# Kernel optimization log

Hardware: AMD Instinct MI355X
Metric: run time of the kernel (lower is better)

Reference implementation:

```python
import jax, jax.numpy as jnp
import numpy as np

PAD_IND = 3
SOS_IND = 0
NSTEPS = 25
H = 256   # hidden_size
D = 256   # input_size (embedding dim)
L = 3     # lstm_layers


def _lstm_cell(x, h, c, Wih, Whh, bih, bhh):
    # torch LSTM gate order: i, f, g, o
    g = x @ Wih.T + bih + h @ Whh.T + bhh
    i, f, gg, o = jnp.split(g, 4, axis=-1)
    c2 = jax.nn.sigmoid(f) * c + jax.nn.sigmoid(i) * jnp.tanh(gg)
    h2 = jax.nn.sigmoid(o) * jnp.tanh(c2)
    return h2, c2


def setup_inputs() -> dict:
    key = jax.random.key(0)
    ks = jax.random.split(key, 24)
    B, T = 64, 256
    Vin, C = 32000, 32000
    s = 1.0 / np.sqrt(H)

    def u(k, shape):
        return jax.random.uniform(k, shape, jnp.float32, -s, s)

    return dict(
        x=jax.random.randint(ks[0], (B, T), 0, Vin),
        target_val=jax.random.randint(ks[1], (B, NSTEPS), 0, C),
        enc_embed=jax.random.normal(ks[2], (Vin, D), jnp.float32),
        enc_Wih=u(ks[3], (L, 4 * H, D)),
        enc_Whh=u(ks[4], (L, 4 * H, H)),
        enc_bih=u(ks[5], (L, 4 * H)),
        enc_bhh=u(ks[6], (L, 4 * H)),
        Wq=u(ks[7], (H, H)), bq=u(ks[8], (H,)),
        Wk=u(ks[9], (H, H)), bk=u(ks[10], (H,)),
        Wv=u(ks[11], (H, H)), bv=u(ks[12], (H,)),
        Wo=u(ks[13], (H, H)), bo=u(ks[14], (H,)),
        dec_embed=jax.random.normal(ks[15], (C, D), jnp.float32),
        dec_Wih0=u(ks[16], (4 * H, 2 * H)),            # decoder layer 0 input is [emb; ctx] = 2H
        dec_Wih_rest=u(ks[17], (L - 1, 4 * H, H)),
        dec_Whh=u(ks[18], (L, 4 * H, H)),
        dec_bih=u(ks[19], (L, 4 * H)),
        dec_bhh=u(ks[20], (L, 4 * H)),
        dec_W=u(ks[21], (C, H)),
        dec_b=u(ks[22], (C,)),
    )


def reference(x, target_val, enc_embed, enc_Wih, enc_Whh, enc_bih, enc_bhh,
              Wq, bq, Wk, bk, Wv, bv, Wo, bo,
              dec_embed, dec_Wih0, dec_Wih_rest, dec_Whh, dec_bih, dec_bhh,
              dec_W, dec_b):
    B, T = x.shape
    lengths = (x != PAD_IND).sum(axis=1)            # [B], emulates pack_padded_sequence
    emb = enc_embed[x]                              # [B,T,D]
    valid = (jnp.arange(T)[:, None] < lengths[None, :])[..., None]  # [T,B,1]
    h0 = jnp.zeros((L, B, H), emb.dtype)
    c0 = jnp.zeros((L, B, H), emb.dtype)

    def enc_step(carry, inp):
        h, c = carry
        xt, v = inp
        hs, cs = [], []
        z = xt
        for l in range(L):
            hl, cl = _lstm_cell(z, h[l], c[l], enc_Wih[l], enc_Whh[l], enc_bih[l], enc_bhh[l])
            hl = jnp.where(v, hl, h[l])             # freeze state past sequence length
            cl = jnp.where(v, cl, c[l])
            hs.append(hl); cs.append(cl)
            z = hl
        h = jnp.stack(hs); c = jnp.stack(cs)
        return (h, c), jnp.where(v, h[-1], 0.0)     # pad_packed pads with zeros

    (enc_h, enc_c), outs = jax.lax.scan(enc_step, (h0, c0), (jnp.swapaxes(emb, 0, 1), valid))
    enc_hiddens = jnp.swapaxes(outs, 0, 1)          # [B,T,H]

    # attention key/value projections are loop-invariant -> hoist out of decode loop
    kp = enc_hiddens @ Wk.T + bk                    # [B,T,H]
    vp = enc_hiddens @ Wv.T + bv                    # [B,T,H]
    scale = 1.0 / jnp.sqrt(jnp.asarray(H, emb.dtype))
    dec_Wih = [dec_Wih0, dec_Wih_rest[0], dec_Wih_rest[1]]
    tok0 = jnp.full((B,), SOS_IND, jnp.int32)

    def dec_step(carry, _):
        h, c, tok = carry
        e = dec_embed[tok]                          # [B,D]
        q = h.sum(axis=0) @ Wq.T + bq               # prev_state[0].sum(axis=0) -> [B,H]
        scores = jnp.einsum('bh,bth->bt', q, kp) * scale
        attn = jax.nn.softmax(scores, axis=-1)
        ctx = jnp.einsum('bt,bth->bh', attn, vp) @ Wo.T + bo
        z = jnp.concatenate([e, ctx], axis=-1)      # [B,2H]
        hs, cs = [], []
        for l in range(L):
            hl, cl = _lstm_cell(z, h[l], c[l], dec_Wih[l], dec_Whh[l], dec_bih[l], dec_bhh[l])
            hs.append(hl); cs.append(cl)
            z = hl
        h = jnp.stack(hs); c = jnp.stack(cs)
        logits = z @ dec_W.T + dec_b                # [B,C]
        tok = jnp.argmax(logits, axis=-1).astype(jnp.int32)  # greedy feedback (TF ratio = 0)
        return (h, c, tok), logits

    _, logits = jax.lax.scan(dec_step, (enc_h, enc_c, tok0), None, length=NSTEPS)  # [25,B,C]
    return jnp.swapaxes(logits, 0, 1)[:, :, None, :]  # [B,25,1,C] like the torch module
```

## Files before the change

kernel.cpp:

```cpp
#include <hip/hip_runtime.h>
#include <math.h>

#define TT    256
#define NB    64
#define HH    256
#define NSTEP 25
#define NCLS  32000
#define PADI  3

__device__ __align__(16) float g_hring[3][2][NB][HH];
__device__ __align__(16) float g_enchid[TT][NB][HH];
__device__ __align__(16) float g_kp[NB][TT][HH];
__device__ __align__(16) float g_vp[NB][TT][HH];
__device__ __align__(16) float g_cfin[3][NB][HH];
__device__ __align__(16) float g_hdec[2][3][NB][HH];
__device__ __align__(16) float g_z0[NB][512];
__device__ float    g_wmax[256][NB];
__device__ int      g_wmaxi[256][NB];
__device__ int      g_len[NB];
__device__ unsigned g_arrive[256];
__device__ unsigned g_release;

__global__ void k_zero_flags(){
  g_arrive[threadIdx.x] = 0u;
  if (threadIdx.x == 0) g_release = 0u;
}

__device__ __forceinline__ float sigf(float v){ return 1.0f / (1.0f + expf(-v)); }

#define SCOPE_AG __HIP_MEMORY_SCOPE_AGENT
typedef unsigned long long u64;
__device__ __forceinline__ float2 ld2(const float* p){
  u64 v = __hip_atomic_load((const u64*)p, __ATOMIC_RELAXED, SCOPE_AG);
  float2 r; __builtin_memcpy(&r, &v, 8); return r;
}
__device__ __forceinline__ void st2(float* p, float2 f){
  u64 v; __builtin_memcpy(&v, &f, 8);
  __hip_atomic_store((u64*)p, v, __ATOMIC_RELAXED, SCOPE_AG);
}
__device__ __forceinline__ float ldc(const float* p){ return __hip_atomic_load(p, __ATOMIC_RELAXED, SCOPE_AG); }
__device__ __forceinline__ void  stc(float* p, float v){ __hip_atomic_store(p, v, __ATOMIC_RELAXED, SCOPE_AG); }
__device__ __forceinline__ int   ldi(const int* p){ return __hip_atomic_load(p, __ATOMIC_RELAXED, SCOPE_AG); }
__device__ __forceinline__ void  sti(int* p, int v){ __hip_atomic_store(p, v, __ATOMIC_RELAXED, SCOPE_AG); }
__device__ __forceinline__ unsigned ldu(const unsigned* p){ return __hip_atomic_load(p, __ATOMIC_RELAXED, SCOPE_AG); }
__device__ __forceinline__ void  stu(unsigned* p, unsigned v){ __hip_atomic_store(p, v, __ATOMIC_RELAXED, SCOPE_AG); }

#define DOT4(a_, x_, w_) (a_) += (x_).x*(w_).x + (x_).y*(w_).y + (x_).z*(w_).z + (x_).w*(w_).w

#define WENC(cb,g,jj,u) (((((cb)*12+(g))*8+(jj))*36)+(u))

__device__ __forceinline__ void gbar(int w, unsigned target){
  asm volatile("s_waitcnt vmcnt(0)" ::: "memory");
  __syncthreads();
  if (threadIdx.x == 0) stu(&g_arrive[w], target);
  if (w == 0){
    if (threadIdx.x < 64){
      const int i4 = threadIdx.x * 4;
      for (;;){
        unsigned a0 = ldu(&g_arrive[i4+0]);
        unsigned a1 = ldu(&g_arrive[i4+1]);
        unsigned a2 = ldu(&g_arrive[i4+2]);
        unsigned a3 = ldu(&g_arrive[i4+3]);
        if (__all((a0>=target) && (a1>=target) && (a2>=target) && (a3>=target))) break;
        __builtin_amdgcn_s_sleep(1);
      }
      if (threadIdx.x == 0) stu(&g_release, target);
    }
  } else {
    if (threadIdx.x == 0){
      while (ldu(&g_release) < target) __builtin_amdgcn_s_sleep(2);
    }
  }
  __syncthreads();
}

template<int NCB, int BASE>
__device__ __forceinline__ void dec_gates(const float* sw, const float* i0, const float* i1,
                                          const float* i2, int j, float out4[4]){
  float a0=0.f, a1=0.f, a2=0.f, a3=0.f;
  const float* ips[3] = { i0, i1, i2 };
  #pragma unroll
  for (int cb = 0; cb < NCB; ++cb){
    float2 xin[16];
    #pragma unroll
    for (int u = 0; u < 16; ++u) xin[u] = ld2(ips[cb] + u*16 + 2*j);
    #pragma unroll
    for (int u2 = 0; u2 < 8; ++u2){
      float2 pa = xin[2*u2], pb = xin[2*u2+1];
      const float* wb = &sw[BASE + (((cb*4+0)*8+j)*36) + u2*4];
      float4 w0 = *(const float4*)(wb);
      float4 w1 = *(const float4*)(wb + 288);
      float4 w2 = *(const float4*)(wb + 576);
      float4 w3 = *(const float4*)(wb + 864);
      a0 += pa.x*w0.x + pa.y*w0.y + pb.x*w0.z + pb.y*w0.w;
      a1 += pa.x*w1.x + pa.y*w1.y + pb.x*w1.z + pb.y*w1.w;
      a2 += pa.x*w2.x + pa.y*w2.y + pb.x*w2.z + pb.y*w2.w;
      a3 += pa.x*w3.x + pa.y*w3.y + pb.x*w3.z + pb.y*w3.w;
    }
  }
  #pragma unroll
  for (int m = 1; m < 8; m <<= 1){
    a0 += __shfl_xor(a0, m); a1 += __shfl_xor(a1, m);
    a2 += __shfl_xor(a2, m); a3 += __shfl_xor(a3, m);
  }
  out4[0]=a0; out4[1]=a1; out4[2]=a2; out4[3]=a3;
}

__global__ void __launch_bounds__(512, 1)
k_main(const int*   __restrict__ p_x,
       const float* __restrict__ p_eemb,
       const float* __restrict__ p_eWih,  const float* __restrict__ p_eWhh,
       const float* __restrict__ p_ebih,  const float* __restrict__ p_ebhh,
       const float* __restrict__ p_Wq, const float* __restrict__ p_bq,
       const float* __restrict__ p_Wk, const float* __restrict__ p_bk,
       const float* __restrict__ p_Wv, const float* __restrict__ p_bv,
       const float* __restrict__ p_Wo, const float* __restrict__ p_bo,
       const float* __restrict__ p_demb,
       const float* __restrict__ p_dWih0, const float* __restrict__ p_dWihR,
       const float* __restrict__ p_dWhh,
       const float* __restrict__ p_dbih,  const float* __restrict__ p_dbhh,
       const float* __restrict__ p_dW,    const float* __restrict__ p_db,
       float* __restrict__ p_out)
{
  __shared__ __align__(16) float s_w[8064];
  __shared__ __align__(16) float s_h2[NB*HH];
  __shared__ float s_benc[12];
  __shared__ float s_bdec[12];
  __shared__ __align__(16) float s_hs[256];
  __shared__ __align__(16) float s_q[256];
  __shared__ __align__(16) float s_sc[256];
  __shared__ __align__(16) float s_at[256];
  __shared__ __align__(16) float s_ctx[256];
  __shared__ float s_rv[8];  __shared__ int s_ri[8];
  __shared__ float s_rv2[8][16]; __shared__ int s_ri2[8][16];

  const int w   = blockIdx.x;
  const int tid = threadIdx.x;
  const int b   = tid >> 3;
  const int j   = tid & 7;
  unsigned bar  = 0;

  const int lay0 = (w < 255) ? (w / 85) : 0;
  const int h0   = (w < 255) ? ((w - lay0*85) * 3) : 0;

  for (int fi = tid; fi < 6144; fi += 512){
    int g = fi >> 9, k = fi & 511;
    int e = g >> 2, gt = g & 3;
    int l   = (w < 255) ? lay0 : e;
    int hh2 = (w < 255) ? (h0 + e) : 255;
    int row = gt*256 + hh2;
    float v = (k < 256) ? p_eWih[((size_t)l*1024 + row)*256 + k]
                        : p_eWhh[((size_t)l*1024 + row)*256 + (k - 256)];
    int cb = k >> 8, kk = k & 255;
    s_w[WENC(cb, g, (kk & 15) >> 1, ((kk >> 4) << 1) | (kk & 1))] = v;
  }
  if (tid < 12){
    int e = tid >> 2, gt = tid & 3;
    int l   = (w < 255) ? lay0 : e;
    int hh2 = (w < 255) ? (h0 + e) : 255;
    int row = gt*256 + hh2;
    s_benc[tid] = p_ebih[l*1024 + row] + p_ebhh[l*1024 + row];
  }
  if (w < 64){
    int cnt = 0;
    if (tid < 256) cnt = (p_x[w*TT + tid] != PADI) ? 1 : 0;
    #pragma unroll
    for (int m = 1; m < 64; m <<= 1) cnt += __shfl_xor(cnt, m);
    if ((tid & 63) == 0) s_ri[tid >> 6] = cnt;
    __syncthreads();
    if (tid == 0){ int t2 = 0; for (int q2 = 0; q2 < 8; ++q2) t2 += s_ri[q2]; sti(&g_len[w], t2); }
  }
  if (tid < 192){
    int fi = w*192 + tid;
    int l = fi >> 14, rem = fi & 16383;
    stc(&g_hring[l][1][rem >> 8][rem & 255], 0.f);
  }
  gbar(w, ++bar);

  const int len_b = ldi(&g_len[b]);

  float c_reg[3] = {0.f,0.f,0.f};
  float h_reg[3] = {0.f,0.f,0.f};

  for (int sdiag = 0; sdiag < TT + 2; ++sdiag){
    float acc[12];
    #pragma unroll
    for (int g = 0; g < 12; ++g) acc[g] = 0.f;

    if (w < 255){
      const int t = sdiag - lay0;
      if (t >= 0 && t < TT){
        float2 x2[16], h2[16];
        if (lay0 == 0){
          const float* xs = p_eemb + (size_t)p_x[b*TT + t]*HH;
          #pragma unroll
          for (int u = 0; u < 16; ++u) x2[u] = *(const float2*)(xs + u*16 + 2*j);
        } else {
          const float* xs = &g_hring[lay0-1][t & 1][b][0];
          #pragma unroll
          for (int u = 0; u < 16; ++u) x2[u] = ld2(xs + u*16 + 2*j);
        }
        {
          const float* hsv = &g_hring[lay0][(t & 1) ^ 1][b][0];
          #pragma unroll
          for (int u = 0; u < 16; ++u) h2[u] = ld2(hsv + u*16 + 2*j);
        }
        #pragma unroll
        for (int u2 = 0; u2 < 8; ++u2){
          float2 xa = x2[2*u2], xb = x2[2*u2+1];
          float2 ha = h2[2*u2], hb = h2[2*u2+1];
          #pragma unroll
          for (int g = 0; g < 12; ++g){
            float4 wx = *(const float4*)&s_w[WENC(0, g, j, u2*4)];
            float4 wh = *(const float4*)&s_w[WENC(1, g, j, u2*4)];
            acc[g] += xa.x*wx.x + xa.y*wx.y + xb.x*wx.z + xb.y*wx.w
                    + ha.x*wh.x + ha.y*wh.y + hb.x*wh.z + hb.y*wh.w;
          }
        }
      }
    } else {
      #pragma unroll
      for (int e = 0; e < 3; ++e){
        const int t = sdiag - e;
        if (t >= 0 && t < TT){
          float2 x2[16], h2[16];
          if (e == 0){
            const float* xs = p_eemb + (size_t)p_x[b*TT + t]*HH;
            #pragma unroll
            for (int u = 0; u < 16; ++u) x2[u] = *(const float2*)(xs + u*16 + 2*j);
          } else {
            const float* xs = &g_hring[e-1][t & 1][b][0];
            #pragma unroll
            for (int u = 0; u < 16; ++u) x2[u] = ld2(xs + u*16 + 2*j);
          }
          {
            const float* hsv = &g_hring[e][(t & 1) ^ 1][b][0];
            #pragma unroll
            for (int u = 0; u < 16; ++u) h2[u] = ld2(hsv + u*16 + 2*j);
          }
          #pragma unroll
          for (int u2 = 0; u2 < 8; ++u2){
            float2 xa = x2[2*u2], xb = x2[2*u2+1];
            float2 ha = h2[2*u2], hb = h2[2*u2+1];
            #pragma unroll
            for (int g2 = 0; g2 < 4; ++g2){
              float4 wx = *(const float4*)&s_w[WENC(0, e*4+g2, j, u2*4)];
              float4 wh = *(const float4*)&s_w[WENC(1, e*4+g2, j, u2*4)];
              acc[e*4+g2] += xa.x*wx.x + xa.y*wx.y + xb.x*wx.z + xb.y*wx.w
                           + ha.x*wh.x + ha.y*wh.y + hb.x*wh.z + hb.y*wh.w;
            }
          }
        }
      }
    }

    #pragma unroll
    for (int g = 0; g < 12; ++g){
      float v = acc[g];
      v += __shfl_xor(v, 1); v += __shfl_xor(v, 2); v += __shfl_xor(v, 4);
      acc[g] = v;
    }

    if (j == 0){
      #pragma unroll
      for (int e = 0; e < 3; ++e){
        const int lay = (w < 255) ? lay0 : e;
        const int hh2 = (w < 255) ? (h0 + e) : 255;
        const int t = sdiag - lay;
        if (t >= 0 && t < TT){
          float iv = acc[e*4+0] + s_benc[e*4+0];
          float fv = acc[e*4+1] + s_benc[e*4+1];
          float gv = acc[e*4+2] + s_benc[e*4+2];
          float ov = acc[e*4+3] + s_benc[e*4+3];
          float c2 = sigf(fv)*c_reg[e] + sigf(iv)*tanhf(gv);
          float h2v = sigf(ov)*tanhf(c2);
          bool valid = (t < len_b);
          if (valid){ c_reg[e] = c2; h_reg[e] = h2v; }
          stc(&g_hring[lay][t & 1][b][hh2], h_reg[e]);
          if (lay == 2) stc(&g_enchid[t][b][hh2], valid ? h_reg[e] : 0.f);
        }
      }
    }
    gbar(w, ++bar);
  }

  if (j == 0){
    #pragma unroll
    for (int e = 0; e < 3; ++e){
      const int lay = (w < 255) ? lay0 : e;
      const int hh2 = (w < 255) ? (h0 + e) : 255;
      stc(&g_cfin[lay][b][hh2], c_reg[e]);
    }
  }
  gbar(w, ++bar);

  {
    const int b2 = w >> 2, t0 = (w & 3) * 64;
    const int n1 = tid & 127, rq = tid >> 7;
    for (int p = 0; p < 4; ++p){
      const int n = p*128 + n1;
      const float* wrow = (n < 256) ? (p_Wk + (size_t)n*HH) : (p_Wv + (size_t)(n-256)*HH);
      const float bias  = (n < 256) ? p_bk[n] : p_bv[n-256];
      const float4* wr4 = (const float4*)wrow;
      const float* hb = &g_enchid[t0 + rq*16][b2][0];
      const float4* hr[16];
      #pragma unroll
      for (int r = 0; r < 16; ++r) hr[r] = (const float4*)(hb + (size_t)r*NB*HH);
      float a16[16];
      #pragma unroll
      for (int r = 0; r < 16; ++r) a16[r] = 0.f;
      for (int k4 = 0; k4 < 64; ++k4){
        float4 wv = wr4[k4];
        #pragma unroll
        for (int r = 0; r < 16; ++r){ float4 h4 = hr[r][k4]; DOT4(a16[r], h4, wv); }
      }
      float* orow = (n < 256) ? &g_kp[b2][t0 + rq*16][n] : &g_vp[b2][t0 + rq*16][n-256];
      #pragma unroll
      for (int r = 0; r < 16; ++r) stc(orow + (size_t)r*HH, a16[r] + bias);
    }
  }

  for (int fi = tid; fi < 3072; fi += 512){
    int g = fi / 768, k = fi % 768; int row = g*256 + w;
    float v = (k < 512) ? p_dWih0[(size_t)row*512 + k]
                        : p_dWhh[(size_t)row*HH + (k - 512)];
    int cb = k >> 8, kk = k & 255;
    s_w[(((cb*4 + g)*8 + ((kk & 15) >> 1))*36) + (((kk >> 4) << 1) | (kk & 1))] = v;
  }
  for (int fi = tid; fi < 2048; fi += 512){
    int g = fi / 512, k = fi % 512; int row = g*256 + w;
    float v = (k < 256) ? p_dWihR[(size_t)row*HH + k]
                        : p_dWhh[(size_t)(1024 + row)*HH + (k - 256)];
    int cb = k >> 8, kk = k & 255;
    s_w[3456 + (((cb*4 + g)*8 + ((kk & 15) >> 1))*36) + (((kk >> 4) << 1) | (kk & 1))] = v;
  }
  for (int fi = tid; fi < 2048; fi += 512){
    int g = fi / 512, k = fi % 512; int row = g*256 + w;
    float v = (k < 256) ? p_dWihR[(size_t)(1024 + row)*HH + k]
                        : p_dWhh[(size_t)(2048 + row)*HH + (k - 256)];
    int cb = k >> 8, kk = k & 255;
    s_w[5760 + (((cb*4 + g)*8 + ((kk & 15) >> 1))*36) + (((kk >> 4) << 1) | (kk & 1))] = v;
  }
  if (tid < 12){
    int l = tid >> 2, g = tid & 3; int row = g*256 + w;
    s_bdec[tid] = p_dbih[l*1024 + row] + p_dbhh[l*1024 + row];
  }
  gbar(w, ++bar);

  if (tid < 192){
    int fi = w*192 + tid;
    int l = fi >> 14, rem = fi & 16383;
    stc(&g_hdec[0][l][rem >> 8][rem & 255], ldc(&g_hring[l][1][rem >> 8][rem & 255]));
  }
  float c_d0 = 0.f, c_d1 = 0.f, c_d2 = 0.f;
  if (j == 0){
    c_d0 = ldc(&g_cfin[0][b][w]); c_d1 = ldc(&g_cfin[1][b][w]); c_d2 = ldc(&g_cfin[2][b][w]);
  }
  gbar(w, ++bar);

  for (int st = 0; st < NSTEP; ++st){
    const int slot = st & 1, nxt = slot ^ 1;

    if (w < 64){
      const int bA = w;
      int tok = 0;
      if (st > 0){
        float v = -1e38f; int idx = 0;
        if (tid < 256){ v = ldc(&g_wmax[tid][bA]); idx = ldi(&g_wmaxi[tid][bA]); }
        #pragma unroll
        for (int m = 1; m < 64; m <<= 1){
          float ov = __shfl_xor(v, m); int oi = __shfl_xor(idx, m);
          if (ov > v || (ov == v && oi < idx)){ v = ov; idx = oi; }
        }
        if ((tid & 63) == 0){ s_rv[tid >> 6] = v; s_ri[tid >> 6] = idx; }
        __syncthreads();
        if (tid == 0){
          float bv2 = s_rv[0]; int bi2 = s_ri[0];
          for (int q2 = 1; q2 < 8; ++q2){
            float ov = s_rv[q2]; int oi = s_ri[q2];
            if (ov > bv2 || (ov == bv2 && oi < bi2)){ bv2 = ov; bi2 = oi; }
          }
          s_ri[0] = bi2;
        }
        __syncthreads();
        tok = s_ri[0];
      }
      if (tid < 256)
        s_hs[tid] = ldc(&g_hdec[slot][0][bA][tid]) + ldc(&g_hdec[slot][1][bA][tid])
                  + ldc(&g_hdec[slot][2][bA][tid]);
      __syncthreads();
      if (tid < 256){
        float a = p_bq[tid];
        const float4* wr = (const float4*)(p_Wq + (size_t)tid*HH);
        #pragma unroll 8
        for (int k4 = 0; k4 < 64; ++k4){
          float4 wv = wr[k4]; float4 h4 = *(const float4*)&s_hs[k4*4]; DOT4(a, h4, wv);
        }
        s_q[tid] = a;
      }
      __syncthreads();
      if (tid < 256){
        float a = 0.f;
        const float4* kr = (const float4*)&g_kp[bA][tid][0];
        #pragma unroll 8
        for (int k4 = 0; k4 < 64; ++k4){
          float4 kv = kr[k4]; float4 q4 = *(const float4*)&s_q[k4*4]; DOT4(a, q4, kv);
        }
        s_sc[tid] = a * 0.0625f;
      }
      __syncthreads();
      {
        float sv = (tid < 256) ? s_sc[tid] : -1e38f;
        float m2 = sv;
        #pragma unroll
        for (int m = 1; m < 64; m <<= 1) m2 = fmaxf(m2, __shfl_xor(m2, m));
        if ((tid & 63) == 0) s_rv[tid >> 6] = m2;
        __syncthreads();
        if (tid == 0){ float mm = s_rv[0]; for (int q2 = 1; q2 < 8; ++q2) mm = fmaxf(mm, s_rv[q2]); s_rv[0] = mm; }
        __syncthreads();
        const float mx = s_rv[0];
        float ev = (tid < 256) ? expf(sv - mx) : 0.f;
        float ss = ev;
        #pragma unroll
        for (int m = 1; m < 64; m <<= 1) ss += __shfl_xor(ss, m);
        __syncthreads();
        if ((tid & 63) == 0) s_rv[tid >> 6] = ss;
        __syncthreads();
        if (tid == 0){ float t2 = 0.f; for (int q2 = 0; q2 < 8; ++q2) t2 += s_rv[q2]; s_rv[0] = t2; }
        __syncthreads();
        if (tid < 256) s_at[tid] = ev / s_rv[0];
      }
      __syncthreads();
      if (tid < 256){
        float a = 0.f;
        const float* vb = &g_vp[bA][0][tid];
        #pragma unroll 4
        for (int t4 = 0; t4 < 64; ++t4){
          float4 a4 = *(const float4*)&s_at[t4*4];
          a += a4.x*vb[(size_t)(t4*4+0)*HH] + a4.y*vb[(size_t)(t4*4+1)*HH]
             + a4.z*vb[(size_t)(t4*4+2)*HH] + a4.w*vb[(size_t)(t4*4+3)*HH];
        }
        s_ctx[tid] = a;
      }
      __syncthreads();
      if (tid < 256){
        float a = p_bo[tid];
        const float4* wr = (const float4*)(p_Wo + (size_t)tid*HH);
        #pragma unroll 8
        for (int k4 = 0; k4 < 64; ++k4){
          float4 wv = wr[k4]; float4 c4 = *(const float4*)&s_ctx[k4*4]; DOT4(a, c4, wv);
        }
        stc(&g_z0[bA][256 + tid], a);
        stc(&g_z0[bA][tid], p_demb[(size_t)tok*HH + tid]);
      }
    }
    gbar(w, ++bar);

    {
      float g4[4];
      dec_gates<3, 0>(s_w, &g_z0[b][0], &g_z0[b][256], &g_hdec[slot][0][b][0], j, g4);
      if (j == 0){
        float iv = g4[0]+s_bdec[0], fv = g4[1]+s_bdec[1], gv = g4[2]+s_bdec[2], ov = g4[3]+s_bdec[3];
        float c2 = sigf(fv)*c_d0 + sigf(iv)*tanhf(gv); c_d0 = c2;
        stc(&g_hdec[nxt][0][b][w], sigf(ov)*tanhf(c2));
      }
    }
    gbar(w, ++bar);
    {
      float g4[4];
      dec_gates<2, 3456>(s_w, &g_hdec[nxt][0][b][0], &g_hdec[slot][1][b][0], nullptr, j, g4);
      if (j == 0){
        float iv = g4[0]+s_bdec[4], fv = g4[1]+s_bdec[5], gv = g4[2]+s_bdec[6], ov = g4[3]+s_bdec[7];
        float c2 = sigf(fv)*c_d1 + sigf(iv)*tanhf(gv); c_d1 = c2;
        stc(&g_hdec[nxt][1][b][w], sigf(ov)*tanhf(c2));
      }
    }
    gbar(w, ++bar);
    {
      float g4[4];
      dec_gates<2, 5760>(s_w, &g_hdec[nxt][1][b][0], &g_hdec[slot][2][b][0], nullptr, j, g4);
      if (j == 0){
        float iv = g4[0]+s_bdec[8], fv = g4[1]+s_bdec[9], gv = g4[2]+s_bdec[10], ov = g4[3]+s_bdec[11];
        float c2 = sigf(fv)*c_d2 + sigf(iv)*tanhf(gv); c_d2 = c2;
        stc(&g_hdec[nxt][2][b][w], sigf(ov)*tanhf(c2));
      }
    }
    gbar(w, ++bar);

    {
      {
        const float* src = &g_hdec[nxt][2][0][0];
        #pragma unroll
        for (int u = 0; u < 16; ++u){
          int fo = 2*(tid + 512*u);
          float2 v = ld2(src + fo);
          *(float2*)(s_h2 + fo) = v;
        }
      }
      __syncthreads();

      const int cq = tid & 127, qb = tid >> 7;
      const bool cok = (cq < 125);
      const int c  = w*125 + cq;
      const int cc = cok ? c : (w*125);
      const float4* wr = (const float4*)(p_dW + (size_t)cc*HH);
      const float4* zr[16];
      #pragma unroll
      for (int r = 0; r < 16; ++r) zr[r] = (const float4*)&s_h2[(qb*16 + r)*HH];
      float a16[16];
      #pragma unroll
      for (int r = 0; r < 16; ++r) a16[r] = 0.f;
      for (int k4 = 0; k4 < 64; ++k4){
        float4 wv = wr[k4];
        #pragma unroll
        for (int r = 0; r < 16; ++r){ float4 z4 = zr[r][k4]; DOT4(a16[r], z4, wv); }
      }
      const float bias = cok ? p_db[cc] : 0.f;
      #pragma unroll
      for (int r = 0; r < 16; ++r){
        const int bb = qb*16 + r;
        float val = a16[r] + bias;
        if (cok) p_out[((size_t)bb*NSTEP + st)*NCLS + c] = val;
        float v = cok ? val : -1e38f;
        int idx = cok ? c : 0x7fffffff;
        #pragma unroll
        for (int m = 1; m < 64; m <<= 1){
          float ov = __shfl_xor(v, m); int oi = __shfl_xor(idx, m);
          if (ov > v || (ov == v && oi < idx)){ v = ov; idx = oi; }
        }
        if ((tid & 63) == 0){ s_rv2[tid >> 6][r] = v; s_ri2[tid >> 6][r] = idx; }
      }
      __syncthreads();
      if (tid < 64){
        const int qb2 = tid >> 4, r = tid & 15;
        float v1 = s_rv2[qb2*2][r];   int i1 = s_ri2[qb2*2][r];
        float v2 = s_rv2[qb2*2+1][r]; int i2 = s_ri2[qb2*2+1][r];
        bool take2 = (v2 > v1) || (v2 == v1 && i2 < i1);
        stc(&g_wmax[w][qb2*16 + r],  take2 ? v2 : v1);
        sti(&g_wmaxi[w][qb2*16 + r], take2 ? i2 : i1);
      }
      __syncthreads();
    }
    gbar(w, ++bar);
  }
}

extern "C" void kernel_launch(void* const* d_in, const int* in_sizes, int n_in,
                              void* d_out, int out_size, void* d_ws, size_t ws_size,
                              hipStream_t stream){
  (void)in_sizes; (void)n_in; (void)out_size; (void)d_ws; (void)ws_size;
  const int*   x     = (const int*)d_in[0];
  const float* eemb  = (const float*)d_in[2];
  const float* eWih  = (const float*)d_in[3];
  const float* eWhh  = (const float*)d_in[4];
  const float* ebih  = (const float*)d_in[5];
  const float* ebhh  = (const float*)d_in[6];
  const float* Wq    = (const float*)d_in[7];
  const float* bq    = (const float*)d_in[8];
  const float* Wk    = (const float*)d_in[9];
  const float* bk    = (const float*)d_in[10];
  const float* Wv    = (const float*)d_in[11];
  const float* bv    = (const float*)d_in[12];
  const float* Wo    = (const float*)d_in[13];
  const float* bo    = (const float*)d_in[14];
  const float* demb  = (const float*)d_in[15];
  const float* dWih0 = (const float*)d_in[16];
  const float* dWihR = (const float*)d_in[17];
  const float* dWhh  = (const float*)d_in[18];
  const float* dbih  = (const float*)d_in[19];
  const float* dbhh  = (const float*)d_in[20];
  const float* dW    = (const float*)d_in[21];
  const float* db    = (const float*)d_in[22];
  float* out = (float*)d_out;

  k_zero_flags<<<dim3(1), dim3(256), 0, stream>>>();
  k_main<<<dim3(256), dim3(512), 0, stream>>>(
      x, eemb, eWih, eWhh, ebih, ebhh,
      Wq, bq, Wk, bk, Wv, bv, Wo, bo,
      demb, dWih0, dWihR, dWhh, dbih, dbhh, dW, db, out);
}
```

Before: 5.994 ms.

## Register-block encoder cells over two batches and rebalance output projection tiling

The encoder recurrence now gives each thread two batch rows and 16 k-lanes, so every shared-memory weight float4 is reused across two batches. Weights are stored in a plain contiguous layout, and the 768 hidden-unit slots are split evenly across blocks, so blocks at a layer boundary can straddle two layers. The decoder output projection computes two classes by eight batch rows per thread and reduces the argmax within a wavefront, which removes the LDS reduction stage and two syncthreads. The barrier spin sleep is also shortened, and the change adds shuffle steps and register pressure in exchange.

```diff
diff --git a/kernel.cpp b/kernel.cpp
--- a/kernel.cpp
+++ b/kernel.cpp
@@ -34,10 +34,6 @@
   u64 v = __hip_atomic_load((const u64*)p, __ATOMIC_RELAXED, SCOPE_AG);
   float2 r; __builtin_memcpy(&r, &v, 8); return r;
 }
-__device__ __forceinline__ void st2(float* p, float2 f){
-  u64 v; __builtin_memcpy(&v, &f, 8);
-  __hip_atomic_store((u64*)p, v, __ATOMIC_RELAXED, SCOPE_AG);
-}
 __device__ __forceinline__ float ldc(const float* p){ return __hip_atomic_load(p, __ATOMIC_RELAXED, SCOPE_AG); }
 __device__ __forceinline__ void  stc(float* p, float v){ __hip_atomic_store(p, v, __ATOMIC_RELAXED, SCOPE_AG); }
 __device__ __forceinline__ int   ldi(const int* p){ return __hip_atomic_load(p, __ATOMIC_RELAXED, SCOPE_AG); }
@@ -46,8 +42,6 @@
 __device__ __forceinline__ void  stu(unsigned* p, unsigned v){ __hip_atomic_store(p, v, __ATOMIC_RELAXED, SCOPE_AG); }
 
 #define DOT4(a_, x_, w_) (a_) += (x_).x*(w_).x + (x_).y*(w_).y + (x_).z*(w_).z + (x_).w*(w_).w
-
-#define WENC(cb,g,jj,u) (((((cb)*12+(g))*8+(jj))*36)+(u))
 
 __device__ __forceinline__ void gbar(int w, unsigned target){
   asm volatile("s_waitcnt vmcnt(0)" ::: "memory");
@@ -68,7 +62,7 @@
     }
   } else {
     if (threadIdx.x == 0){
-      while (ldu(&g_release) < target) __builtin_amdgcn_s_sleep(2);
+      while (ldu(&g_release) < target) __builtin_amdgcn_s_sleep(1);
     }
   }
   __syncthreads();
@@ -132,7 +126,6 @@
   __shared__ __align__(16) float s_at[256];
   __shared__ __align__(16) float s_ctx[256];
   __shared__ float s_rv[8];  __shared__ int s_ri[8];
-  __shared__ float s_rv2[8][16]; __shared__ int s_ri2[8][16];
 
   const int w   = blockIdx.x;
   const int tid = threadIdx.x;
@@ -140,25 +133,26 @@
   const int j   = tid & 7;
   unsigned bar  = 0;
 
-  const int lay0 = (w < 255) ? (w / 85) : 0;
-  const int h0   = (w < 255) ? ((w - lay0*85) * 3) : 0;
+  const int b2  = tid >> 4;
+  const int je  = tid & 15;
+  const int slot3 = 3*w;
+  const int layU  = slot3 >> 8;
+  const bool uni  = ((slot3 + 2) >> 8) == layU;
 
   for (int fi = tid; fi < 6144; fi += 512){
-    int g = fi >> 9, k = fi & 511;
-    int e = g >> 2, gt = g & 3;
-    int l   = (w < 255) ? lay0 : e;
-    int hh2 = (w < 255) ? (h0 + e) : 255;
-    int row = gt*256 + hh2;
-    float v = (k < 256) ? p_eWih[((size_t)l*1024 + row)*256 + k]
-                        : p_eWhh[((size_t)l*1024 + row)*256 + (k - 256)];
-    int cb = k >> 8, kk = k & 255;
-    s_w[WENC(cb, g, (kk & 15) >> 1, ((kk >> 4) << 1) | (kk & 1))] = v;
+    int cb = fi / 3072, rem = fi - cb*3072;
+    int g = rem >> 8, k = rem & 255;
+    int s3 = slot3 + (g >> 2);
+    int l = s3 >> 8, hh = s3 & 255;
+    int row = (g & 3)*256 + hh;
+    float v = (cb == 0) ? p_eWih[((size_t)l*1024 + row)*256 + k]
+                        : p_eWhh[((size_t)l*1024 + row)*256 + k];
+    s_w[fi] = v;
   }
   if (tid < 12){
-    int e = tid >> 2, gt = tid & 3;
-    int l   = (w < 255) ? lay0 : e;
-    int hh2 = (w < 255) ? (h0 + e) : 255;
-    int row = gt*256 + hh2;
+    int s3 = slot3 + (tid >> 2);
+    int l = s3 >> 8, hh = s3 & 255;
+    int row = (tid & 3)*256 + hh;
     s_benc[tid] = p_ebih[l*1024 + row] + p_ebhh[l*1024 + row];
   }
   if (w < 64){
@@ -177,77 +171,113 @@
   }
   gbar(w, ++bar);
 
-  const int len_b = ldi(&g_len[b]);
-
-  float c_reg[3] = {0.f,0.f,0.f};
-  float h_reg[3] = {0.f,0.f,0.f};
+  const int len0 = ldi(&g_len[2*b2]);
+  const int len1 = ldi(&g_len[2*b2+1]);
+
+  float c_reg[3][2] = {{0.f,0.f},{0.f,0.f},{0.f,0.f}};
+  float h_reg[3][2] = {{0.f,0.f},{0.f,0.f},{0.f,0.f}};
 
   for (int sdiag = 0; sdiag < TT + 2; ++sdiag){
-    float acc[12];
+    float acc[12][2];
     #pragma unroll
-    for (int g = 0; g < 12; ++g) acc[g] = 0.f;
-
-    if (w < 255){
-      const int t = sdiag - lay0;
+    for (int g = 0; g < 12; ++g){ acc[g][0] = 0.f; acc[g][1] = 0.f; }
+
+    if (uni){
+      const int t = sdiag - layU;
       if (t >= 0 && t < TT){
-        float2 x2[16], h2[16];
-        if (lay0 == 0){
-          const float* xs = p_eemb + (size_t)p_x[b*TT + t]*HH;
+        float4 xv[2][4], hv[2][4];
+        #pragma unroll
+        for (int bb = 0; bb < 2; ++bb){
+          const int batch = 2*b2 + bb;
+          const float* hs = &g_hring[layU][(t & 1) ^ 1][batch][0];
+          if (layU == 0){
+            const float* xs = p_eemb + (size_t)p_x[batch*TT + t]*HH;
+            #pragma unroll
+            for (int u = 0; u < 4; ++u){
+              int off = 64*u + 4*je;
+              float2 a = *(const float2*)(xs + off);
+              float2 c = *(const float2*)(xs + off + 2);
+              xv[bb][u] = make_float4(a.x, a.y, c.x, c.y);
+            }
+          } else {
+            const float* xs = &g_hring[layU-1][t & 1][batch][0];
+            #pragma unroll
+            for (int u = 0; u < 4; ++u){
+              int off = 64*u + 4*je;
+              float2 a = ld2(xs + off), c = ld2(xs + off + 2);
+              xv[bb][u] = make_float4(a.x, a.y, c.x, c.y);
+            }
+          }
           #pragma unroll
-          for (int u = 0; u < 16; ++u) x2[u] = *(const float2*)(xs + u*16 + 2*j);
-        } else {
-          const float* xs = &g_hring[lay0-1][t & 1][b][0];
-          #pragma unroll
-          for (int u = 0; u < 16; ++u) x2[u] = ld2(xs + u*16 + 2*j);
-        }
-        {
-          const float* hsv = &g_hring[lay0][(t & 1) ^ 1][b][0];
-          #pragma unroll
-          for (int u = 0; u < 16; ++u) h2[u] = ld2(hsv + u*16 + 2*j);
-        }
-        #pragma unroll
-        for (int u2 = 0; u2 < 8; ++u2){
-          float2 xa = x2[2*u2], xb = x2[2*u2+1];
-          float2 ha = h2[2*u2], hb = h2[2*u2+1];
+          for (int u = 0; u < 4; ++u){
+            int off = 64*u + 4*je;
+            float2 a = ld2(hs + off), c = ld2(hs + off + 2);
+            hv[bb][u] = make_float4(a.x, a.y, c.x, c.y);
+          }
+        }
+        #pragma unroll
+        for (int u = 0; u < 4; ++u){
           #pragma unroll
           for (int g = 0; g < 12; ++g){
-            float4 wx = *(const float4*)&s_w[WENC(0, g, j, u2*4)];
-            float4 wh = *(const float4*)&s_w[WENC(1, g, j, u2*4)];
-            acc[g] += xa.x*wx.x + xa.y*wx.y + xb.x*wx.z + xb.y*wx.w
-                    + ha.x*wh.x + ha.y*wh.y + hb.x*wh.z + hb.y*wh.w;
+            float4 wx = *(const float4*)&s_w[g*256 + 64*u + 4*je];
+            float4 wh = *(const float4*)&s_w[3072 + g*256 + 64*u + 4*je];
+            #pragma unroll
+            for (int bb = 0; bb < 2; ++bb){
+              DOT4(acc[g][bb], xv[bb][u], wx);
+              DOT4(acc[g][bb], hv[bb][u], wh);
+            }
           }
         }
       }
     } else {
       #pragma unroll
       for (int e = 0; e < 3; ++e){
-        const int t = sdiag - e;
+        const int s3 = slot3 + e;
+        const int lay = s3 >> 8;
+        const int t = sdiag - lay;
         if (t >= 0 && t < TT){
-          float2 x2[16], h2[16];
-          if (e == 0){
-            const float* xs = p_eemb + (size_t)p_x[b*TT + t]*HH;
+          float4 xv[2][4], hv[2][4];
+          #pragma unroll
+          for (int bb = 0; bb < 2; ++bb){
+            const int batch = 2*b2 + bb;
+            const float* hs = &g_hring[lay][(t & 1) ^ 1][batch][0];
+            if (lay == 0){
+              const float* xs = p_eemb + (size_t)p_x[batch*TT + t]*HH;
+              #pragma unroll
+              for (int u = 0; u < 4; ++u){
+                int off = 64*u + 4*je;
+                float2 a = *(const float2*)(xs + off);
+                float2 c = *(const float2*)(xs + off + 2);
+                xv[bb][u] = make_float4(a.x, a.y, c.x, c.y);
+              }
+            } else {
+              const float* xs = &g_hring[lay-1][t & 1][batch][0];
+              #pragma unroll
+              for (int u = 0; u < 4; ++u){
+                int off = 64*u + 4*je;
+                float2 a = ld2(xs + off), c = ld2(xs + off + 2);
+                xv[bb][u] = make_float4(a.x, a.y, c.x, c.y);
+              }
+            }
             #pragma unroll
-            for (int u = 0; u < 16; ++u) x2[u] = *(const float2*)(xs + u*16 + 2*j);
-          } else {
-            const float* xs = &g_hring[e-1][t & 1][b][0];
-            #pragma unroll
-            for (int u = 0; u < 16; ++u) x2[u] = ld2(xs + u*16 + 2*j);
-          }
-          {
-            const float* hsv = &g_hring[e][(t & 1) ^ 1][b][0];
-            #pragma unroll
-            for (int u = 0; u < 16; ++u) h2[u] = ld2(hsv + u*16 + 2*j);
+            for (int u = 0; u < 4; ++u){
+              int off = 64*u + 4*je;
+              float2 a = ld2(hs + off), c = ld2(hs + off + 2);
+              hv[bb][u] = make_float4(a.x, a.y, c.x, c.y);
+            }
           }
           #pragma unroll
-          for (int u2 = 0; u2 < 8; ++u2){
-            float2 xa = x2[2*u2], xb = x2[2*u2+1];
-            float2 ha = h2[2*u2], hb = h2[2*u2+1];
+          for (int u = 0; u < 4; ++u){
             #pragma unroll
-            for (int g2 = 0; g2 < 4; ++g2){
-              float4 wx = *(const float4*)&s_w[WENC(0, e*4+g2, j, u2*4)];
-              float4 wh = *(const float4*)&s_w[WENC(1, e*4+g2, j, u2*4)];
-              acc[e*4+g2] += xa.x*wx.x + xa.y*wx.y + xb.x*wx.z + xb.y*wx.w
-                           + ha.x*wh.x + ha.y*wh.y + hb.x*wh.z + hb.y*wh.w;
+            for (int gt = 0; gt < 4; ++gt){
+              int g = e*4 + gt;
+              float4 wx = *(const float4*)&s_w[g*256 + 64*u + 4*je];
+              float4 wh = *(const float4*)&s_w[3072 + g*256 + 64*u + 4*je];
+              #pragma unroll
+              for (int bb = 0; bb < 2; ++bb){
+                DOT4(acc[g][bb], xv[bb][u], wx);
+                DOT4(acc[g][bb], hv[bb][u], wh);
+              }
             }
           }
         }
@@ -256,53 +286,62 @@
 
     #pragma unroll
     for (int g = 0; g < 12; ++g){
-      float v = acc[g];
-      v += __shfl_xor(v, 1); v += __shfl_xor(v, 2); v += __shfl_xor(v, 4);
-      acc[g] = v;
-    }
-
-    if (j == 0){
+      #pragma unroll
+      for (int bb = 0; bb < 2; ++bb){
+        float v = acc[g][bb];
+        v += __shfl_xor(v, 1); v += __shfl_xor(v, 2);
+        v += __shfl_xor(v, 4); v += __shfl_xor(v, 8);
+        acc[g][bb] = v;
+      }
+    }
+
+    if (je == 0){
       #pragma unroll
       for (int e = 0; e < 3; ++e){
-        const int lay = (w < 255) ? lay0 : e;
-        const int hh2 = (w < 255) ? (h0 + e) : 255;
+        const int s3 = slot3 + e;
+        const int lay = s3 >> 8, hh = s3 & 255;
         const int t = sdiag - lay;
         if (t >= 0 && t < TT){
-          float iv = acc[e*4+0] + s_benc[e*4+0];
-          float fv = acc[e*4+1] + s_benc[e*4+1];
-          float gv = acc[e*4+2] + s_benc[e*4+2];
-          float ov = acc[e*4+3] + s_benc[e*4+3];
-          float c2 = sigf(fv)*c_reg[e] + sigf(iv)*tanhf(gv);
-          float h2v = sigf(ov)*tanhf(c2);
-          bool valid = (t < len_b);
-          if (valid){ c_reg[e] = c2; h_reg[e] = h2v; }
-          stc(&g_hring[lay][t & 1][b][hh2], h_reg[e]);
-          if (lay == 2) stc(&g_enchid[t][b][hh2], valid ? h_reg[e] : 0.f);
+          #pragma unroll
+          for (int bb = 0; bb < 2; ++bb){
+            const int batch = 2*b2 + bb;
+            float iv = acc[e*4+0][bb] + s_benc[e*4+0];
+            float fv = acc[e*4+1][bb] + s_benc[e*4+1];
+            float gv = acc[e*4+2][bb] + s_benc[e*4+2];
+            float ov = acc[e*4+3][bb] + s_benc[e*4+3];
+            float c2 = sigf(fv)*c_reg[e][bb] + sigf(iv)*tanhf(gv);
+            float h2v = sigf(ov)*tanhf(c2);
+            bool valid = (t < ((bb == 0) ? len0 : len1));
+            if (valid){ c_reg[e][bb] = c2; h_reg[e][bb] = h2v; }
+            stc(&g_hring[lay][t & 1][batch][hh], h_reg[e][bb]);
+            if (lay == 2) stc(&g_enchid[t][batch][hh], valid ? h_reg[e][bb] : 0.f);
+          }
         }
       }
     }
     gbar(w, ++bar);
   }
 
-  if (j == 0){
+  if (je == 0){
     #pragma unroll
     for (int e = 0; e < 3; ++e){
-      const int lay = (w < 255) ? lay0 : e;
-      const int hh2 = (w < 255) ? (h0 + e) : 255;
-      stc(&g_cfin[lay][b][hh2], c_reg[e]);
+      const int s3 = slot3 + e;
+      const int lay = s3 >> 8, hh = s3 & 255;
+      stc(&g_cfin[lay][2*b2][hh],   c_reg[e][0]);
+      stc(&g_cfin[lay][2*b2+1][hh], c_reg[e][1]);
     }
   }
   gbar(w, ++bar);
 
   {
-    const int b2 = w >> 2, t0 = (w & 3) * 64;
+    const int b3 = w >> 2, t0 = (w & 3) * 64;
     const int n1 = tid & 127, rq = tid >> 7;
     for (int p = 0; p < 4; ++p){
       const int n = p*128 + n1;
       const float* wrow = (n < 256) ? (p_Wk + (size_t)n*HH) : (p_Wv + (size_t)(n-256)*HH);
       const float bias  = (n < 256) ? p_bk[n] : p_bv[n-256];
       const float4* wr4 = (const float4*)wrow;
-      const float* hb = &g_enchid[t0 + rq*16][b2][0];
+      const float* hb = &g_enchid[t0 + rq*16][b3][0];
       const float4* hr[16];
       #pragma unroll
       for (int r = 0; r < 16; ++r) hr[r] = (const float4*)(hb + (size_t)r*NB*HH);
@@ -314,7 +353,7 @@
         #pragma unroll
         for (int r = 0; r < 16; ++r){ float4 h4 = hr[r][k4]; DOT4(a16[r], h4, wv); }
       }
-      float* orow = (n < 256) ? &g_kp[b2][t0 + rq*16][n] : &g_vp[b2][t0 + rq*16][n-256];
+      float* orow = (n < 256) ? &g_kp[b3][t0 + rq*16][n] : &g_vp[b3][t0 + rq*16][n-256];
       #pragma unroll
       for (int r = 0; r < 16; ++r) stc(orow + (size_t)r*HH, a16[r] + bias);
     }
@@ -499,47 +538,46 @@
       }
       __syncthreads();
 
-      const int cq = tid & 127, qb = tid >> 7;
-      const bool cok = (cq < 125);
-      const int c  = w*125 + cq;
-      const int cc = cok ? c : (w*125);
-      const float4* wr = (const float4*)(p_dW + (size_t)cc*HH);
-      const float4* zr[16];
-      #pragma unroll
-      for (int r = 0; r < 16; ++r) zr[r] = (const float4*)&s_h2[(qb*16 + r)*HH];
-      float a16[16];
-      #pragma unroll
-      for (int r = 0; r < 16; ++r) a16[r] = 0.f;
+      const int cs = tid & 63, qb = tid >> 6;
+      const bool ok0 = (2*cs)   < 125;
+      const bool ok1 = (2*cs+1) < 125;
+      const int c0 = w*125 + 2*cs, c1 = c0 + 1;
+      const float4* wr0 = (const float4*)(p_dW + (size_t)(ok0 ? c0 : w*125)*HH);
+      const float4* wr1 = (const float4*)(p_dW + (size_t)(ok1 ? c1 : w*125)*HH);
+      const float4* zr[8];
+      #pragma unroll
+      for (int r = 0; r < 8; ++r) zr[r] = (const float4*)&s_h2[(qb*8 + r)*HH];
+      float a0[8], a1[8];
+      #pragma unroll
+      for (int r = 0; r < 8; ++r){ a0[r] = 0.f; a1[r] = 0.f; }
       for (int k4 = 0; k4 < 64; ++k4){
-        float4 wv = wr[k4];
-        #pragma unroll
-        for (int r = 0; r < 16; ++r){ float4 z4 = zr[r][k4]; DOT4(a16[r], z4, wv); }
-      }
-      const float bias = cok ? p_db[cc] : 0.f;
-      #pragma unroll
-      for (int r = 0; r < 16; ++r){
-        const int bb = qb*16 + r;
-        float val = a16[r] + bias;
-        if (cok) p_out[((size_t)bb*NSTEP + st)*NCLS + c] = val;
-        float v = cok ? val : -1e38f;
-        int idx = cok ? c : 0x7fffffff;
+        float4 w0 = wr0[k4], w1 = wr1[k4];
+        #pragma unroll
+        for (int r = 0; r < 8; ++r){
+          float4 z4 = zr[r][k4];
+          DOT4(a0[r], z4, w0);
+          DOT4(a1[r], z4, w1);
+        }
+      }
+      const float bias0 = ok0 ? p_db[c0] : 0.f;
+      const float bias1 = ok1 ? p_db[c1] : 0.f;
+      #pragma unroll
+      for (int r = 0; r < 8; ++r){
+        const int bb = qb*8 + r;
+        float val0 = a0[r] + bias0, val1 = a1[r] + bias1;
+        float* orow = p_out + ((size_t)bb*NSTEP + st)*NCLS;
+        if (ok0) orow[c0] = val0;
+        if (ok1) orow[c1] = val1;
+        float v = ok0 ? val0 : -1e38f;
+        int idx  = ok0 ? c0 : 0x7fffffff;
+        if (ok1 && val1 > v){ v = val1; idx = c1; }
         #pragma unroll
         for (int m = 1; m < 64; m <<= 1){
           float ov = __shfl_xor(v, m); int oi = __shfl_xor(idx, m);
           if (ov > v || (ov == v && oi < idx)){ v = ov; idx = oi; }
         }
-        if ((tid & 63) == 0){ s_rv2[tid >> 6][r] = v; s_ri2[tid >> 6][r] = idx; }
-      }
-      __syncthreads();
-      if (tid < 64){
-        const int qb2 = tid >> 4, r = tid & 15;
-        float v1 = s_rv2[qb2*2][r];   int i1 = s_ri2[qb2*2][r];
-        float v2 = s_rv2[qb2*2+1][r]; int i2 = s_ri2[qb2*2+1][r];
-        bool take2 = (v2 > v1) || (v2 == v1 && i2 < i1);
-        stc(&g_wmax[w][qb2*16 + r],  take2 ? v2 : v1);
-        sti(&g_wmaxi[w][qb2*16 + r], take2 ? i2 : i1);
-      }
-      __syncthreads();
+        if (cs == 0){ stc(&g_wmax[w][bb], v); sti(&g_wmaxi[w][bb], idx); }
+      }
     }
     gbar(w, ++bar);
   }
```

After: 7.077 ms. 1.18x slower.

## Spread barrier release flags across lines and restructure output-projection tiling

Applied to the files above, without the earlier changes.

The grid barrier's single release word is replaced by 16 release flags, one per cache line, each polled by 16 workgroups, so fewer blocks contend on one address. Waiters also spin with a shorter sleep. The logits projection now has each thread compute two classes for 8 batch rows instead of one class for 16 rows, and each wavefront owns whole rows. This lets the argmax reduction finish inside the wavefront and removes the shared-memory merge and its two __syncthreads. The cost is doubled global weight-row loads per thread and a possible change in coalescing of the output stores.

```diff
diff --git a/kernel.cpp b/kernel.cpp
--- a/kernel.cpp
+++ b/kernel.cpp
@@ -19,11 +19,11 @@
 __device__ int      g_wmaxi[256][NB];
 __device__ int      g_len[NB];
 __device__ unsigned g_arrive[256];
-__device__ unsigned g_release;
+__device__ unsigned g_rel[256];
 
 __global__ void k_zero_flags(){
   g_arrive[threadIdx.x] = 0u;
-  if (threadIdx.x == 0) g_release = 0u;
+  g_rel[threadIdx.x] = 0u;
 }
 
 __device__ __forceinline__ float sigf(float v){ return 1.0f / (1.0f + expf(-v)); }
@@ -33,10 +33,6 @@
 __device__ __forceinline__ float2 ld2(const float* p){
   u64 v = __hip_atomic_load((const u64*)p, __ATOMIC_RELAXED, SCOPE_AG);
   float2 r; __builtin_memcpy(&r, &v, 8); return r;
-}
-__device__ __forceinline__ void st2(float* p, float2 f){
-  u64 v; __builtin_memcpy(&v, &f, 8);
-  __hip_atomic_store((u64*)p, v, __ATOMIC_RELAXED, SCOPE_AG);
 }
 __device__ __forceinline__ float ldc(const float* p){ return __hip_atomic_load(p, __ATOMIC_RELAXED, SCOPE_AG); }
 __device__ __forceinline__ void  stc(float* p, float v){ __hip_atomic_store(p, v, __ATOMIC_RELAXED, SCOPE_AG); }
@@ -64,11 +60,12 @@
         if (__all((a0>=target) && (a1>=target) && (a2>=target) && (a3>=target))) break;
         __builtin_amdgcn_s_sleep(1);
       }
-      if (threadIdx.x == 0) stu(&g_release, target);
+      if (threadIdx.x < 16) stu(&g_rel[threadIdx.x << 4], target);
     }
   } else {
     if (threadIdx.x == 0){
-      while (ldu(&g_release) < target) __builtin_amdgcn_s_sleep(2);
+      const unsigned* line = &g_rel[(w >> 4) << 4];
+      while (ldu(line) < target) __builtin_amdgcn_s_sleep(1);
     }
   }
   __syncthreads();
@@ -132,7 +129,6 @@
   __shared__ __align__(16) float s_at[256];
   __shared__ __align__(16) float s_ctx[256];
   __shared__ float s_rv[8];  __shared__ int s_ri[8];
-  __shared__ float s_rv2[8][16]; __shared__ int s_ri2[8][16];
 
   const int w   = blockIdx.x;
   const int tid = threadIdx.x;
@@ -295,14 +291,14 @@
   gbar(w, ++bar);
 
   {
-    const int b2 = w >> 2, t0 = (w & 3) * 64;
+    const int b3 = w >> 2, t0 = (w & 3) * 64;
     const int n1 = tid & 127, rq = tid >> 7;
     for (int p = 0; p < 4; ++p){
       const int n = p*128 + n1;
       const float* wrow = (n < 256) ? (p_Wk + (size_t)n*HH) : (p_Wv + (size_t)(n-256)*HH);
       const float bias  = (n < 256) ? p_bk[n] : p_bv[n-256];
       const float4* wr4 = (const float4*)wrow;
-      const float* hb = &g_enchid[t0 + rq*16][b2][0];
+      const float* hb = &g_enchid[t0 + rq*16][b3][0];
       const float4* hr[16];
       #pragma unroll
       for (int r = 0; r < 16; ++r) hr[r] = (const float4*)(hb + (size_t)r*NB*HH);
@@ -314,7 +310,7 @@
         #pragma unroll
         for (int r = 0; r < 16; ++r){ float4 h4 = hr[r][k4]; DOT4(a16[r], h4, wv); }
       }
-      float* orow = (n < 256) ? &g_kp[b2][t0 + rq*16][n] : &g_vp[b2][t0 + rq*16][n-256];
+      float* orow = (n < 256) ? &g_kp[b3][t0 + rq*16][n] : &g_vp[b3][t0 + rq*16][n-256];
       #pragma unroll
       for (int r = 0; r < 16; ++r) stc(orow + (size_t)r*HH, a16[r] + bias);
     }
@@ -499,47 +495,46 @@
       }
       __syncthreads();
 
-      const int cq = tid & 127, qb = tid >> 7;
-      const bool cok = (cq < 125);
-      const int c  = w*125 + cq;
-      const int cc = cok ? c : (w*125);
-      const float4* wr = (const float4*)(p_dW + (size_t)cc*HH);
-      const float4* zr[16];
-      #pragma unroll
-      for (int r = 0; r < 16; ++r) zr[r] = (const float4*)&s_h2[(qb*16 + r)*HH];
-      float a16[16];
-      #pragma unroll
-      for (int r = 0; r < 16; ++r) a16[r] = 0.f;
+      const int cs = tid & 63, qb = tid >> 6;
+      const bool ok0 = (2*cs)   < 125;
+      const bool ok1 = (2*cs+1) < 125;
+      const int c0 = w*125 + 2*cs, c1 = c0 + 1;
+      const float4* wr0 = (const float4*)(p_dW + (size_t)(ok0 ? c0 : w*125)*HH);
+      const float4* wr1 = (const float4*)(p_dW + (size_t)(ok1 ? c1 : w*125)*HH);
+      const float4* zr[8];
+      #pragma unroll
+      for (int r = 0; r < 8; ++r) zr[r] = (const float4*)&s_h2[(qb*8 + r)*HH];
+      float a0[8], a1[8];
+      #pragma unroll
+      for (int r = 0; r < 8; ++r){ a0[r] = 0.f; a1[r] = 0.f; }
       for (int k4 = 0; k4 < 64; ++k4){
-        float4 wv = wr[k4];
-        #pragma unroll
-        for (int r = 0; r < 16; ++r){ float4 z4 = zr[r][k4]; DOT4(a16[r], z4, wv); }
-      }
-      const float bias = cok ? p_db[cc] : 0.f;
-      #pragma unroll
-      for (int r = 0; r < 16; ++r){
-        const int bb = qb*16 + r;
-        float val = a16[r] + bias;
-        if (cok) p_out[((size_t)bb*NSTEP + st)*NCLS + c] = val;
-        float v = cok ? val : -1e38f;
-        int idx = cok ? c : 0x7fffffff;
+        float4 w0 = wr0[k4], w1 = wr1[k4];
+        #pragma unroll
+        for (int r = 0; r < 8; ++r){
+          float4 z4 = zr[r][k4];
+          DOT4(a0[r], z4, w0);
+          DOT4(a1[r], z4, w1);
+        }
+      }
+      const float bias0 = ok0 ? p_db[c0] : 0.f;
+      const float bias1 = ok1 ? p_db[c1] : 0.f;
+      #pragma unroll
+      for (int r = 0; r < 8; ++r){
+        const int bb = qb*8 + r;
+        float val0 = a0[r] + bias0, val1 = a1[r] + bias1;
+        float* orow = p_out + ((size_t)bb*NSTEP + st)*NCLS;
+        if (ok0) orow[c0] = val0;
+        if (ok1) orow[c1] = val1;
+        float v = ok0 ? val0 : -1e38f;
+        int idx  = ok0 ? c0 : 0x7fffffff;
+        if (ok1 && val1 > v){ v = val1; idx = c1; }
         #pragma unroll
         for (int m = 1; m < 64; m <<= 1){
           float ov = __shfl_xor(v, m); int oi = __shfl_xor(idx, m);
           if (ov > v || (ov == v && oi < idx)){ v = ov; idx = oi; }
         }
-        if ((tid & 63) == 0){ s_rv2[tid >> 6][r] = v; s_ri2[tid >> 6][r] = idx; }
-      }
-      __syncthreads();
-      if (tid < 64){
-        const int qb2 = tid >> 4, r = tid & 15;
-        float v1 = s_rv2[qb2*2][r];   int i1 = s_ri2[qb2*2][r];
-        float v2 = s_rv2[qb2*2+1][r]; int i2 = s_ri2[qb2*2+1][r];
-        bool take2 = (v2 > v1) || (v2 == v1 && i2 < i1);
-        stc(&g_wmax[w][qb2*16 + r],  take2 ? v2 : v1);
-        sti(&g_wmaxi[w][qb2*16 + r], take2 ? i2 : i1);
-      }
-      __syncthreads();
+        if (cs == 0){ stc(&g_wmax[w][bb], v); sti(&g_wmaxi[w][bb], idx); }
+      }
     }
     gbar(w, ++bar);
   }
```

Result: faster. 5.863 ms (-2.2%).
